# Kernel tuning notes

Measured on AMD Instinct MI355X. Metric: run time of the kernel, lower is better.

## Reference

```python
import jax, jax.numpy as jnp
import numpy as np

B, T, C = 2, 2048, 1024
NUM_HEADS, NUM_KV_HEADS, HEAD_DIM = 16, 8, 64
R = NUM_HEADS // NUM_KV_HEADS  # q heads per kv head
WINDOW = 512
HIDDEN = 4096
SOFT_CAP = 50.0


def setup_inputs() -> dict:
    key = jax.random.key(0)
    ks = jax.random.split(key, 10)
    std = 0.02
    return {
        "x": jax.random.normal(ks[0], (B, T, C), jnp.float32),
        "kurtosis_sum": jnp.zeros((), jnp.float32),
        "rms1_scale": jnp.zeros((C,), jnp.float32),
        "q_kernel": std * jax.random.normal(ks[1], (C, R, NUM_KV_HEADS, HEAD_DIM), jnp.float32),
        "k_kernel": std * jax.random.normal(ks[2], (C, NUM_KV_HEADS, HEAD_DIM), jnp.float32),
        "v_kernel": std * jax.random.normal(ks[3], (C, NUM_KV_HEADS, HEAD_DIM), jnp.float32),
        "out_kernel": std * jax.random.normal(ks[4], (R, NUM_KV_HEADS, HEAD_DIM, C), jnp.float32),
        "rms2_scale": jnp.zeros((C,), jnp.float32),
        "gate_kernel": std * jax.random.normal(ks[5], (C, HIDDEN), jnp.float32),
        "up_kernel": std * jax.random.normal(ks[6], (C, HIDDEN), jnp.float32),
        "down_kernel": std * jax.random.normal(ks[7], (HIDDEN, C), jnp.float32),
    }


def sine_table(features, length, max_timescale=1e6):
    fraction = jnp.arange(0, features, 2, dtype=jnp.float32) / features
    rot_freq = 1.0 / (max_timescale ** fraction)
    sinusoid = jnp.arange(length, dtype=jnp.float32)[:, None] * rot_freq[None, :]
    sinusoid = jnp.concatenate([sinusoid, sinusoid], axis=-1)  # (T, features)
    return jnp.sin(sinusoid), jnp.cos(sinusoid)


def rotate_half(x):
    x1, x2 = jnp.split(x, 2, axis=-1)
    return jnp.concatenate([-x2, x1], axis=-1)


def rms_norm(x, scale):
    var = jnp.mean(jnp.square(x.astype(jnp.float32)), axis=-1, keepdims=True)
    normed = (x * jax.lax.rsqrt(var + 1e-6)).astype(x.dtype)
    return normed * (1 + scale)


def excess_kurtosis(emb):
    mean = jnp.mean(emb, axis=-1, keepdims=True)
    std = jnp.std(emb, axis=-1, keepdims=True)
    centralized = emb - mean
    fourth = jnp.mean(centralized ** 4, axis=-1, keepdims=True)
    kurt = jnp.squeeze(fourth / (std ** 4 + 1e-6), axis=-1).reshape(-1) - 3
    return jnp.sum(jnp.maximum(kurt, 0.0))


def reference(x, kurtosis_sum, rms1_scale, q_kernel, k_kernel, v_kernel,
              out_kernel, rms2_scale, gate_kernel, up_kernel, down_kernel):
    Bc, Tc, Cc = x.shape
    # sliding-window causal mask: j <= i and |i - j| < WINDOW
    idx = jnp.arange(Tc)
    causal = idx[:, None] >= idx[None, :]
    band = jnp.abs(idx[:, None] - idx[None, :]) < WINDOW
    mask = (causal & band)[None, None, None]  # (1,1,1,T,T) for brhsd scores

    # --- attention ---
    attn_in = rms_norm(x, rms1_scale)
    q = jnp.einsum('bsm,mrhk->brhsk', attn_in, q_kernel)
    k = jnp.einsum('bdm,mhk->bhdk', attn_in, k_kernel)
    v = jnp.einsum('bdm,mhv->bhdv', attn_in, v_kernel)

    sin, cos = sine_table(HEAD_DIM, Tc, max_timescale=1e6)
    q = q * cos[None, None, None] + rotate_half(q) * sin[None, None, None]
    k = k * cos[None, None] + rotate_half(k) * sin[None, None]

    scale = jax.lax.rsqrt(jnp.asarray(HEAD_DIM, dtype=x.dtype))
    qk = jnp.einsum('brhsk,bhdk->brhsd', q, k) * scale
    qk = jnp.tanh(qk / SOFT_CAP) * SOFT_CAP
    probs = jax.nn.softmax(qk.astype(jnp.float32), where=mask).astype(x.dtype)
    qkv = jnp.einsum('brhsd,bhdv->brhsv', probs, v)
    attn_out = jnp.einsum('brhsv,rhvm->bsm', qkv, out_kernel)
    x = x + attn_out

    # --- SwiGLU MLP ---
    mlp_in = rms_norm(x, rms2_scale)
    gate = jax.nn.silu(mlp_in @ gate_kernel)
    up = mlp_in @ up_kernel
    x = x + (up * gate) @ down_kernel

    return (x, kurtosis_sum + excess_kurtosis(x))
```

## Files before the change

### kernel.cpp

```cpp
#include <hip/hip_runtime.h>
#include <hip/hip_bf16.h>

typedef __attribute__((ext_vector_type(8))) short short8;
typedef __attribute__((ext_vector_type(4))) float f32x4;
typedef __attribute__((ext_vector_type(4))) int int4v;
typedef __attribute__((ext_vector_type(8))) int int8v;

#define DEVFN static __device__ __forceinline__

DEVFN float bf2f(unsigned short u) {
    unsigned int i = ((unsigned int)u) << 16;
    float f; __builtin_memcpy(&f, &i, 4); return f;
}
DEVFN unsigned short f2bf(float f) {
    unsigned int i; __builtin_memcpy(&i, &f, 4);
    unsigned int r = i + 0x7fffu + ((i >> 16) & 1u);
    return (unsigned short)(r >> 16);
}
DEVFN unsigned char f2fp8(float f) {
    int r = __builtin_amdgcn_cvt_pk_fp8_f32(f, f, 0, false);
    return (unsigned char)(r & 0xff);
}
DEVFN float fastrcp(float x) { return __builtin_amdgcn_rcpf(x); }

DEVFN void load_lds16(const void* g, void* l) {
    __builtin_amdgcn_global_load_lds(
        (__attribute__((address_space(1))) void*)g,
        (__attribute__((address_space(3))) void*)l, 16, 0, 0);
}

DEVFN f32x4 mfma_fp8(int8v a, int8v b, f32x4 c) {
    return __builtin_amdgcn_mfma_scale_f32_16x16x128_f8f6f4(
        a, b, c, 0, 0, 0, 0x7F7F7F7F, 0, 0x7F7F7F7F);
}

constexpr int Bsz = 2, T = 2048, C = 1024;
constexpr int NH = 16, NKV = 8, HD = 64;
constexpr int HID = 4096;
constexpr int NTOK = Bsz * T;
constexpr size_t MiB = 1024 * 1024;

constexpr size_t OFF_WQKV = 0;
constexpr size_t OFF_WOUT = 4 * MiB;
constexpr size_t OFF_WGATE = 6 * MiB;
constexpr size_t OFF_WUP = 10 * MiB;
constexpr size_t OFF_WDOWN = 14 * MiB;
constexpr size_t OFF_XN1 = 18 * MiB;
constexpr size_t OFF_VBUF = 26 * MiB;
constexpr size_t OFF_P2 = 26 * MiB;
constexpr size_t OFF_QB = 58 * MiB;
constexpr size_t OFF_KB = 66 * MiB;
constexpr size_t OFF_VT = 70 * MiB;
constexpr size_t OFF_CTX = 74 * MiB;
constexpr size_t OFF_X2 = 82 * MiB;
constexpr size_t OFF_XN2 = 98 * MiB;
constexpr size_t OFF_G = 102 * MiB;
constexpr size_t OFF_P4 = 118 * MiB;
constexpr size_t OFF_ST = 134 * MiB;
constexpr size_t OFF_CT = 134 * MiB + 256 * 1024;

__global__ __launch_bounds__(256) void prep_kernel(
    const float* __restrict__ qk, const float* __restrict__ kk2,
    const float* __restrict__ vk, const float* __restrict__ ok,
    const float* __restrict__ gk, const float* __restrict__ uk,
    const float* __restrict__ dk,
    unsigned short* __restrict__ wqkv, unsigned short* __restrict__ wout,
    unsigned char* __restrict__ wgate, unsigned char* __restrict__ wup,
    unsigned char* __restrict__ wdown,
    const float* __restrict__ x, const float* __restrict__ rms1_scale,
    unsigned short* __restrict__ xn1,
    float* __restrict__ st, float* __restrict__ ct) {
    __shared__ float t[32][33];
    __shared__ float red[4];
    int id = blockIdx.x;
    int tid = threadIdx.x;
    if (id >= 19456) {
        int idx = (id - 19456) * 256 + tid;
        float fr = (float)(idx & 31) * (1.f / 32.f);
        float freq = powf(1e6f, -fr);
        float a = (float)(idx >> 5) * freq;
        st[idx] = sinf(a);
        ct[idx] = cosf(a);
        return;
    }
    if (id >= 15360) {
        int row = id - 15360;
        const float4 v = *(const float4*)&x[(size_t)row * 1024 + tid * 4];
        float ss = v.x * v.x + v.y * v.y + v.z * v.z + v.w * v.w;
#pragma unroll
        for (int m = 32; m; m >>= 1) ss += __shfl_xor(ss, m, 64);
        if ((tid & 63) == 0) red[tid >> 6] = ss;
        __syncthreads();
        float tot = red[0] + red[1] + red[2] + red[3];
        float inv = rsqrtf(tot * (1.f / 1024.f) + 1e-6f);
        const float4 sc = *(const float4*)&rms1_scale[tid * 4];
        size_t o = (size_t)row * 1024 + tid * 4;
        xn1[o + 0] = f2bf(v.x * inv * (1.f + sc.x));
        xn1[o + 1] = f2bf(v.y * inv * (1.f + sc.y));
        xn1[o + 2] = f2bf(v.z * inv * (1.f + sc.z));
        xn1[o + 3] = f2bf(v.w * inv * (1.f + sc.w));
        return;
    }
    const float* in; int K, N, nx, base; int fp8 = 0;
    unsigned short* out16 = nullptr; unsigned char* out8 = nullptr;
    if (id < 1024)       { in = qk;  out16 = wqkv;                       K = 1024; N = 1024; nx = 32;  base = 0; }
    else if (id < 1536)  { in = kk2; out16 = wqkv + (size_t)1024 * 1024; K = 1024; N = 512;  nx = 16;  base = 1024; }
    else if (id < 2048)  { in = vk;  out16 = wqkv + (size_t)1536 * 1024; K = 1024; N = 512;  nx = 16;  base = 1536; }
    else if (id < 3072)  { in = ok;  out16 = wout;                       K = 1024; N = 1024; nx = 32;  base = 2048; }
    else if (id < 7168)  { in = gk;  out8 = wgate; fp8 = 1;              K = 1024; N = 4096; nx = 128; base = 3072; }
    else if (id < 11264) { in = uk;  out8 = wup; fp8 = 1;                K = 1024; N = 4096; nx = 128; base = 7168; }
    else                 { in = dk;  out8 = wdown; fp8 = 1;              K = 4096; N = 1024; nx = 32;  base = 11264; }
    int lid = id - base;
    int n0 = (lid % nx) * 32, k0 = (lid / nx) * 32;
    int tx = tid & 31, ty = tid >> 5;
#pragma unroll
    for (int i = 0; i < 4; i++)
        t[ty + 8 * i][tx] = in[(size_t)(k0 + ty + 8 * i) * N + n0 + tx];
    __syncthreads();
    if (fp8) {
#pragma unroll
        for (int i = 0; i < 4; i++)
            out8[(size_t)(n0 + ty + 8 * i) * K + k0 + tx] = f2fp8(t[tx][ty + 8 * i] * 16.f);
    } else {
#pragma unroll
        for (int i = 0; i < 4; i++)
            out16[(size_t)(n0 + ty + 8 * i) * K + k0 + tx] = f2bf(t[tx][ty + 8 * i]);
    }
}

__global__ __launch_bounds__(256) void gemm128(const unsigned short* __restrict__ A,
                                               const unsigned short* __restrict__ Bt,
                                               unsigned short* __restrict__ Cp,
                                               int N, int K, int lda, int ldb,
                                               size_t zA, size_t zB, size_t zC) {
    __shared__ __align__(16) unsigned short As[2][128 * 32];
    __shared__ __align__(16) unsigned short Bs[2][128 * 32];
    A += (size_t)blockIdx.z * zA;
    Bt += (size_t)blockIdx.z * zB;
    const int tid = threadIdx.x;
    const int lane = tid & 63, w = tid >> 6;
    const int quad = lane >> 4, l15 = lane & 15;
    const int wr = w >> 1, wc = w & 1;
    const int m0 = blockIdx.y * 128, n0 = blockIdx.x * 128;

    f32x4 acc[4][4];
#pragma unroll
    for (int i = 0; i < 4; i++)
#pragma unroll
        for (int j = 0; j < 4; j++) acc[i][j] = f32x4{0.f, 0.f, 0.f, 0.f};

    const int stRow = (w << 4) + (lane >> 2);
    const int stCol = (lane & 3) << 3;

    auto STAGE = [&](int kk, int b) {
#pragma unroll
        for (int i = 0; i < 2; i++) {
            load_lds16(A + (size_t)(m0 + (i << 6) + stRow) * lda + kk + stCol,
                       &As[b][((i << 6) + (w << 4)) * 32]);
            load_lds16(Bt + (size_t)(n0 + (i << 6) + stRow) * ldb + kk + stCol,
                       &Bs[b][((i << 6) + (w << 4)) * 32]);
        }
    };

    const int nsteps = K >> 5;
    STAGE(0, 0);
    STAGE(32, 1);
    for (int s = 0; s < nsteps; ++s) {
        if (s < nsteps - 1) asm volatile("s_waitcnt vmcnt(4)\n\ts_barrier" ::: "memory");
        else                asm volatile("s_waitcnt vmcnt(0)\n\ts_barrier" ::: "memory");
        const int b = s & 1;
        short8 a[4], bf[4];
#pragma unroll
        for (int mi = 0; mi < 4; mi++)
            a[mi] = *(const short8*)&As[b][(wr * 64 + mi * 16 + l15) * 32 + quad * 8];
#pragma unroll
        for (int ni = 0; ni < 4; ni++)
            bf[ni] = *(const short8*)&Bs[b][(wc * 64 + ni * 16 + l15) * 32 + quad * 8];
        asm volatile("s_waitcnt lgkmcnt(0)\n\ts_barrier" ::: "memory");
        if (s + 2 < nsteps) STAGE((s + 2) * 32, b);
        __builtin_amdgcn_sched_barrier(0);
        __builtin_amdgcn_s_setprio(1);
#pragma unroll
        for (int mi = 0; mi < 4; mi++)
#pragma unroll
            for (int ni = 0; ni < 4; ni++)
                acc[mi][ni] = __builtin_amdgcn_mfma_f32_16x16x32_bf16(a[mi], bf[ni], acc[mi][ni], 0, 0, 0);
        __builtin_amdgcn_s_setprio(0);
    }
#pragma unroll
    for (int mi = 0; mi < 4; mi++)
#pragma unroll
        for (int ni = 0; ni < 4; ni++)
#pragma unroll
            for (int r = 0; r < 4; r++) {
                int row = m0 + wr * 64 + mi * 16 + quad * 4 + r;
                int col = n0 + wc * 64 + ni * 16 + l15;
                Cp[(size_t)blockIdx.z * zC + (size_t)row * N + col] = f2bf(acc[mi][ni][r]);
            }
}

__global__ __launch_bounds__(256) void gemm_qkv(const unsigned short* __restrict__ A,
                                                const unsigned short* __restrict__ Bt,
                                                unsigned short* __restrict__ qb,
                                                unsigned short* __restrict__ kb,
                                                unsigned short* __restrict__ vbuf,
                                                const float* __restrict__ st,
                                                const float* __restrict__ ct) {
    __shared__ __align__(16) unsigned short As[2][128 * 32];
    __shared__ __align__(16) unsigned short Bs[2][128 * 32];
    const int tid = threadIdx.x;
    const int lane = tid & 63, w = tid >> 6;
    const int quad = lane >> 4, l15 = lane & 15;
    const int wr = w >> 1, wc = w & 1;
    const int m0 = blockIdx.y * 128, n0 = blockIdx.x * 128;

    f32x4 acc[4][4];
#pragma unroll
    for (int i = 0; i < 4; i++)
#pragma unroll
        for (int j = 0; j < 4; j++) acc[i][j] = f32x4{0.f, 0.f, 0.f, 0.f};

    const int stRow = (w << 4) + (lane >> 2);
    const int stCol = (lane & 3) << 3;

    auto STAGE = [&](int kk, int b) {
#pragma unroll
        for (int i = 0; i < 2; i++) {
            load_lds16(A + (size_t)(m0 + (i << 6) + stRow) * 1024 + kk + stCol,
                       &As[b][((i << 6) + (w << 4)) * 32]);
            load_lds16(Bt + (size_t)(n0 + (i << 6) + stRow) * 1024 + kk + stCol,
                       &Bs[b][((i << 6) + (w << 4)) * 32]);
        }
    };

    STAGE(0, 0);
    STAGE(32, 1);
    for (int s = 0; s < 32; ++s) {
        if (s < 31) asm volatile("s_waitcnt vmcnt(4)\n\ts_barrier" ::: "memory");
        else        asm volatile("s_waitcnt vmcnt(0)\n\ts_barrier" ::: "memory");
        const int b = s & 1;
        short8 a[4], bf[4];
#pragma unroll
        for (int mi = 0; mi < 4; mi++)
            a[mi] = *(const short8*)&As[b][(wr * 64 + mi * 16 + l15) * 32 + quad * 8];
#pragma unroll
        for (int ni = 0; ni < 4; ni++)
            bf[ni] = *(const short8*)&Bs[b][(wc * 64 + ni * 16 + l15) * 32 + quad * 8];
        asm volatile("s_waitcnt lgkmcnt(0)\n\ts_barrier" ::: "memory");
        if (s < 30) STAGE((s + 2) * 32, b);
        __builtin_amdgcn_sched_barrier(0);
        __builtin_amdgcn_s_setprio(1);
#pragma unroll
        for (int mi = 0; mi < 4; mi++)
#pragma unroll
            for (int ni = 0; ni < 4; ni++)
                acc[mi][ni] = __builtin_amdgcn_mfma_f32_16x16x32_bf16(a[mi], bf[ni], acc[mi][ni], 0, 0, 0);
        __builtin_amdgcn_s_setprio(0);
    }

    if (n0 < 1536) {
        const int head = (n0 + wc * 64) >> 6;
        const bool isq = head < 16;
        unsigned short* ob = isq ? qb : kb;
        const int hb = isq ? head : head - 16;
        const int hn = isq ? 16 : 8;
#pragma unroll
        for (int ni = 0; ni < 2; ni++) {
            const int d = ni * 16 + l15;
#pragma unroll
            for (int mi = 0; mi < 4; mi++)
#pragma unroll
                for (int r = 0; r < 4; r++) {
                    int row = m0 + wr * 64 + mi * 16 + quad * 4 + r;
                    int t = row & 2047, bb = row >> 11;
                    float c = ct[t * 32 + d], sv = st[t * 32 + d];
                    float x1 = acc[mi][ni][r], x2 = acc[mi][ni + 2][r];
                    size_t obase = ((size_t)(bb * hn + hb) * 2048 + t) * 64;
                    ob[obase + d]      = f2bf(x1 * c - x2 * sv);
                    ob[obase + d + 32] = f2bf(x2 * c + x1 * sv);
                }
        }
    } else {
#pragma unroll
        for (int mi = 0; mi < 4; mi++)
#pragma unroll
            for (int ni = 0; ni < 4; ni++)
#pragma unroll
                for (int r = 0; r < 4; r++) {
                    int row = m0 + wr * 64 + mi * 16 + quad * 4 + r;
                    int col = n0 - 1536 + wc * 64 + ni * 16 + l15;
                    vbuf[(size_t)row * 512 + col] = f2bf(acc[mi][ni][r]);
                }
    }
}

__global__ __launch_bounds__(256) void vtrans_kernel(const unsigned short* __restrict__ vbuf,
                                                     unsigned short* __restrict__ vt) {
    __shared__ unsigned short tile[64][68];
    int lid = blockIdx.x;
    int tid = threadIdx.x;
    int b = lid >> 8, h = (lid >> 5) & 7, t0 = (lid & 31) * 64;
    int d = tid & 63, tr = tid >> 6;
#pragma unroll
    for (int i = 0; i < 16; i++) {
        int t = tr + i * 4;
        tile[t][d] = vbuf[(size_t)(b * 2048 + t0 + t) * 512 + h * 64 + d];
    }
    __syncthreads();
    int tt = tid & 63, dr = tid >> 6;
#pragma unroll
    for (int i = 0; i < 16; i++) {
        int dd = dr + i * 4;
        vt[((size_t)(b * 8 + h) * 64 + dd) * 2048 + t0 + tt] = tile[tt][dd];
    }
}

DEVFN int8v read_frag8(const unsigned char* buf, int rb, int quad) {
    int base = rb * 128;
    int h0 = (2 * quad) ^ (rb & 7);
    int h1 = (2 * quad + 1) ^ (rb & 7);
    int4v lo = *(const int4v*)&buf[base + h0 * 16];
    int4v hi = *(const int4v*)&buf[base + h1 * 16];
    return int8v{lo.x, lo.y, lo.z, lo.w, hi.x, hi.y, hi.z, hi.w};
}

__global__ __launch_bounds__(256) void gateup_kernel(const unsigned char* __restrict__ A,
                                                     const unsigned char* __restrict__ Bg,
                                                     const unsigned char* __restrict__ Bu,
                                                     unsigned char* __restrict__ out) {
    __shared__ __align__(16) unsigned char As[2][128 * 128];
    __shared__ __align__(16) unsigned char Gs[2][64 * 128];
    __shared__ __align__(16) unsigned char Us[2][64 * 128];
    const int tid = threadIdx.x;
    const int lane = tid & 63, w = tid >> 6;
    const int quad = lane >> 4, l15 = lane & 15;
    const int wr = w >> 1, wc = w & 1;
    const int m0 = blockIdx.y * 128, n0 = blockIdx.x * 64;

    f32x4 aG[4][2], aU[4][2];
#pragma unroll
    for (int i = 0; i < 4; i++)
#pragma unroll
        for (int j = 0; j < 2; j++) { aG[i][j] = f32x4{0.f, 0.f, 0.f, 0.f}; aU[i][j] = f32x4{0.f, 0.f, 0.f, 0.f}; }

    const int lrow = lane >> 3;
    const int hA = (lane & 7) ^ lrow;

    auto STAGE = [&](int t, int b) {
#pragma unroll
        for (int j = 0; j < 4; j++) {
            int i = w * 4 + j;
            int r = i * 8 + lrow;
            load_lds16(A + (size_t)(m0 + r) * 1024 + t * 128 + hA * 16, &As[b][i * 1024]);
        }
#pragma unroll
        for (int j = 0; j < 2; j++) {
            int i = w * 2 + j;
            int r = i * 8 + lrow;
            load_lds16(Bg + (size_t)(n0 + r) * 1024 + t * 128 + hA * 16, &Gs[b][i * 1024]);
            load_lds16(Bu + (size_t)(n0 + r) * 1024 + t * 128 + hA * 16, &Us[b][i * 1024]);
        }
    };

    STAGE(0, 0);
    STAGE(1, 1);

#pragma unroll
    for (int t = 0; t < 8; ++t) {
        if (t < 7) asm volatile("s_waitcnt vmcnt(8)\n\ts_barrier" ::: "memory");
        else       asm volatile("s_waitcnt vmcnt(0)\n\ts_barrier" ::: "memory");
        const int b = t & 1;
        int8v a[4], bg[2], bu[2];
#pragma unroll
        for (int mi = 0; mi < 4; mi++)
            a[mi] = read_frag8(As[b], wr * 64 + mi * 16 + l15, quad);
#pragma unroll
        for (int ni = 0; ni < 2; ni++) {
            bg[ni] = read_frag8(Gs[b], wc * 32 + ni * 16 + l15, quad);
            bu[ni] = read_frag8(Us[b], wc * 32 + ni * 16 + l15, quad);
        }
        asm volatile("s_waitcnt lgkmcnt(0)\n\ts_barrier" ::: "memory");
        if (t < 6) STAGE(t + 2, b);
        __builtin_amdgcn_sched_barrier(0);
        __builtin_amdgcn_s_setprio(1);
#pragma unroll
        for (int mi = 0; mi < 4; mi++)
#pragma unroll
            for (int ni = 0; ni < 2; ni++) {
                aG[mi][ni] = mfma_fp8(a[mi], bg[ni], aG[mi][ni]);
                aU[mi][ni] = mfma_fp8(a[mi], bu[ni], aU[mi][ni]);
            }
        __builtin_amdgcn_s_setprio(0);
    }
#pragma unroll
    for (int mi = 0; mi < 4; mi++)
#pragma unroll
        for (int ni = 0; ni < 2; ni++)
#pragma unroll
            for (int r = 0; r < 4; r++) {
                int row = m0 + wr * 64 + mi * 16 + quad * 4 + r;
                int col = n0 + wc * 32 + ni * 16 + l15;
                float vg = aG[mi][ni][r] * (1.f / 64.f);
                float vu = aU[mi][ni][r] * (1.f / 64.f);
                float s = vg * fastrcp(1.f + __expf(-vg));
                out[(size_t)row * 4096 + col] = f2fp8(s * vu * 8.f);
            }
}

__global__ __launch_bounds__(256) void down_gemm(const unsigned char* __restrict__ A,
                                                 const unsigned char* __restrict__ Bt,
                                                 unsigned short* __restrict__ Cp) {
    __shared__ __align__(16) unsigned char As[2][128 * 128];
    __shared__ __align__(16) unsigned char Bs[2][128 * 128];
    const int tid = threadIdx.x;
    const int lane = tid & 63, w = tid >> 6;
    const int quad = lane >> 4, l15 = lane & 15;
    const int wr = w >> 1, wc = w & 1;
    const int m0 = blockIdx.y * 128, n0 = blockIdx.x * 128;
    const int kbase = blockIdx.z * 2048;

    f32x4 acc[4][4];
#pragma unroll
    for (int i = 0; i < 4; i++)
#pragma unroll
        for (int j = 0; j < 4; j++) acc[i][j] = f32x4{0.f, 0.f, 0.f, 0.f};

    const int lrow = lane >> 3;
    const int hA = (lane & 7) ^ lrow;

    auto STAGE = [&](int t, int b) {
#pragma unroll
        for (int j = 0; j < 4; j++) {
            int i = w * 4 + j;
            int r = i * 8 + lrow;
            load_lds16(A + (size_t)(m0 + r) * 4096 + kbase + t * 128 + hA * 16, &As[b][i * 1024]);
            load_lds16(Bt + (size_t)(n0 + r) * 4096 + kbase + t * 128 + hA * 16, &Bs[b][i * 1024]);
        }
    };

    STAGE(0, 0);
    STAGE(1, 1);

#pragma unroll
    for (int t = 0; t < 16; ++t) {
        if (t < 15) asm volatile("s_waitcnt vmcnt(8)\n\ts_barrier" ::: "memory");
        else        asm volatile("s_waitcnt vmcnt(0)\n\ts_barrier" ::: "memory");
        const int b = t & 1;
        int8v a[4], bb[4];
#pragma unroll
        for (int mi = 0; mi < 4; mi++)
            a[mi] = read_frag8(As[b], wr * 64 + mi * 16 + l15, quad);
#pragma unroll
        for (int ni = 0; ni < 4; ni++)
            bb[ni] = read_frag8(Bs[b], wc * 64 + ni * 16 + l15, quad);
        asm volatile("s_waitcnt lgkmcnt(0)\n\ts_barrier" ::: "memory");
        if (t < 14) STAGE(t + 2, b);
        __builtin_amdgcn_sched_barrier(0);
        __builtin_amdgcn_s_setprio(1);
#pragma unroll
        for (int mi = 0; mi < 4; mi++)
#pragma unroll
            for (int ni = 0; ni < 4; ni++)
                acc[mi][ni] = mfma_fp8(a[mi], bb[ni], acc[mi][ni]);
        __builtin_amdgcn_s_setprio(0);
    }
    const size_t Z = (size_t)NTOK * 1024;
#pragma unroll
    for (int mi = 0; mi < 4; mi++)
#pragma unroll
        for (int ni = 0; ni < 4; ni++)
#pragma unroll
            for (int r = 0; r < 4; r++) {
                int row = m0 + wr * 64 + mi * 16 + quad * 4 + r;
                int col = n0 + wc * 64 + ni * 16 + l15;
                Cp[(size_t)blockIdx.z * Z + (size_t)row * 1024 + col] =
                    f2bf(acc[mi][ni][r] * (1.f / 128.f));
            }
}

__global__ __launch_bounds__(256) void reduce_out(const unsigned short* __restrict__ p,
                                                  const float* __restrict__ x,
                                                  const float* __restrict__ scale,
                                                  float* __restrict__ x2,
                                                  unsigned char* __restrict__ xn2,
                                                  const float* __restrict__ ksum,
                                                  float* __restrict__ outk) {
    __shared__ float red[4];
    int row = blockIdx.x, tid = threadIdx.x;
    if (row == 0 && tid == 0) outk[0] = ksum[0];
    size_t base = (size_t)row * 1024 + tid * 4;
    const size_t Z = (size_t)NTOK * 1024;
    float4 v = *(const float4*)&x[base];
#pragma unroll
    for (int z = 0; z < 2; z++) {
        ushort4 u = *(const ushort4*)&p[base + z * Z];
        v.x += bf2f(u.x); v.y += bf2f(u.y); v.z += bf2f(u.z); v.w += bf2f(u.w);
    }
    *(float4*)&x2[base] = v;
    float ss = v.x * v.x + v.y * v.y + v.z * v.z + v.w * v.w;
#pragma unroll
    for (int m = 32; m; m >>= 1) ss += __shfl_xor(ss, m, 64);
    if ((tid & 63) == 0) red[tid >> 6] = ss;
    __syncthreads();
    float tot = red[0] + red[1] + red[2] + red[3];
    float inv = rsqrtf(tot * (1.f / 1024.f) + 1e-6f) * 4.f;
    const float4 sc = *(const float4*)&scale[tid * 4];
    xn2[base + 0] = f2fp8(v.x * inv * (1.f + sc.x));
    xn2[base + 1] = f2fp8(v.y * inv * (1.f + sc.y));
    xn2[base + 2] = f2fp8(v.z * inv * (1.f + sc.z));
    xn2[base + 3] = f2fp8(v.w * inv * (1.f + sc.w));
}

__global__ __launch_bounds__(256) void reduce_down(const unsigned short* __restrict__ p,
                                                   const float* __restrict__ x2,
                                                   float* __restrict__ outx,
                                                   float* __restrict__ outk) {
    __shared__ float red[4], r2[4], r4[4];
    int row = blockIdx.x, tid = threadIdx.x;
    size_t base = (size_t)row * 1024 + tid * 4;
    const size_t Z = (size_t)NTOK * 1024;
    float4 v = *(const float4*)&x2[base];
#pragma unroll
    for (int z = 0; z < 2; z++) {
        ushort4 u = *(const ushort4*)&p[base + z * Z];
        v.x += bf2f(u.x); v.y += bf2f(u.y); v.z += bf2f(u.z); v.w += bf2f(u.w);
    }
    *(float4*)&outx[base] = v;
    float s = v.x + v.y + v.z + v.w;
#pragma unroll
    for (int m = 32; m; m >>= 1) s += __shfl_xor(s, m, 64);
    if ((tid & 63) == 0) red[tid >> 6] = s;
    __syncthreads();
    float mean = (red[0] + red[1] + red[2] + red[3]) * (1.f / 1024.f);
    float cx = v.x - mean, cy = v.y - mean, cz = v.z - mean, cw = v.w - mean;
    float x2v = cx * cx, y2 = cy * cy, z2 = cz * cz, w2 = cw * cw;
    float c2 = x2v + y2 + z2 + w2;
    float c4 = x2v * x2v + y2 * y2 + z2 * z2 + w2 * w2;
#pragma unroll
    for (int m = 32; m; m >>= 1) {
        c2 += __shfl_xor(c2, m, 64);
        c4 += __shfl_xor(c4, m, 64);
    }
    if ((tid & 63) == 0) { r2[tid >> 6] = c2; r4[tid >> 6] = c4; }
    __syncthreads();
    if (tid == 0) {
        float m2 = (r2[0] + r2[1] + r2[2] + r2[3]) * (1.f / 1024.f);
        float m4 = (r4[0] + r4[1] + r4[2] + r4[3]) * (1.f / 1024.f);
        float kurt = m4 / (m2 * m2 + 1e-6f) - 3.f;
        if (kurt > 0.f) atomicAdd(outk, kurt);
    }
}

__global__ __launch_bounds__(256) void attn_kernel(const unsigned short* __restrict__ qb,
                                                   const unsigned short* __restrict__ kb,
                                                   const unsigned short* __restrict__ vt,
                                                   unsigned short* __restrict__ ctx) {
    __shared__ __align__(16) unsigned short Ks[64 * 64];
    __shared__ __align__(16) unsigned short Vs[64 * 64];
    __shared__ __align__(16) unsigned short P[4][2][16 * 64];
    const int tid = threadIdx.x, lane = tid & 63, w = tid >> 6;
    const int quad = lane >> 4, l15 = lane & 15;
    const int qt = blockIdx.x, H = blockIdx.y, b = blockIdx.z;
    const int hkv = H & 7;
    const int qw = qt * 64 + w * 16;

    const unsigned short* qbase = qb + ((size_t)(b * 16 + H) * 2048 + qw) * 64;
    short8 aq0 = *(const short8*)(qbase + (size_t)l15 * 64 + quad * 8);
    short8 aq1 = *(const short8*)(qbase + (size_t)l15 * 64 + 32 + quad * 8);

    const unsigned short* kbase = kb + (size_t)(b * 8 + hkv) * 2048 * 64;
    const unsigned short* vbase = vt + (size_t)(b * 8 + hkv) * 64 * 2048;

    const short bf1 = (short)0x3F80;
    const short8 ones = {bf1, bf1, bf1, bf1, bf1, bf1, bf1, bf1};

    f32x4 O[4];
#pragma unroll
    for (int i = 0; i < 4; i++) O[i] = f32x4{0.f, 0.f, 0.f, 0.f};
    f32x4 lacc = f32x4{0.f, 0.f, 0.f, 0.f};

    const int srow = lane >> 3;
    const int schunk = (lane & 7) ^ srow;
    const int sw = l15 & 7;

    int kstartB = qt * 64 - 511;
    if (kstartB < 0) kstartB = 0;
    kstartB &= ~63;
    const int kendB = qt * 64 + 63;
    int buf = 0;

    for (int k0 = kstartB; k0 <= kendB; k0 += 64) {
#pragma unroll
        for (int rr = 0; rr < 2; rr++) {
            int row = w * 8 + rr * 32 + srow;
            load_lds16(kbase + (size_t)(k0 + row) * 64 + schunk * 8,
                       &Ks[(w * 8 + rr * 32) * 64]);
            load_lds16(vbase + (size_t)row * 2048 + k0 + schunk * 8,
                       &Vs[(w * 8 + rr * 32) * 64]);
        }
        __syncthreads();
        f32x4 S[4];
#pragma unroll
        for (int c = 0; c < 4; c++) {
            const unsigned short* kp = &Ks[(c * 16 + l15) * 64];
            short8 kf0 = *(const short8*)&kp[(quad ^ sw) * 8];
            short8 kf1 = *(const short8*)&kp[((4 + quad) ^ sw) * 8];
            f32x4 s = __builtin_amdgcn_mfma_f32_16x16x32_bf16(aq0, kf0, f32x4{0.f, 0.f, 0.f, 0.f}, 0, 0, 0);
            s = __builtin_amdgcn_mfma_f32_16x16x32_bf16(aq1, kf1, s, 0, 0, 0);
            S[c] = s;
        }
        unsigned short* Pw = P[w][buf];
#pragma unroll
        for (int c = 0; c < 4; c++)
#pragma unroll
            for (int r = 0; r < 4; r++) {
                int i = qw + quad * 4 + r;
                int j = k0 + c * 16 + l15;
                float Sc = fminf(3200.f, fmaxf(-3200.f, S[c][r]));
                float e = __expf(Sc * 0.005f);
                float y = 50.f - 100.f * fastrcp(e + 1.f);
                bool ok = (j <= i) && ((i - j) < 512);
                float pv = ok ? __expf(y) : 0.f;
                Pw[(quad * 4 + r) * 64 + c * 16 + l15] = f2bf(pv);
            }
        asm volatile("s_waitcnt lgkmcnt(0)" ::: "memory");
        short8 pf0 = *(const short8*)&Pw[l15 * 64 + quad * 8];
        short8 pf1 = *(const short8*)&Pw[l15 * 64 + 32 + quad * 8];
#pragma unroll
        for (int ni = 0; ni < 4; ni++) {
            const unsigned short* vp = &Vs[(ni * 16 + l15) * 64];
            short8 vf0 = *(const short8*)&vp[(quad ^ sw) * 8];
            short8 vf1 = *(const short8*)&vp[((4 + quad) ^ sw) * 8];
            O[ni] = __builtin_amdgcn_mfma_f32_16x16x32_bf16(pf0, vf0, O[ni], 0, 0, 0);
            O[ni] = __builtin_amdgcn_mfma_f32_16x16x32_bf16(pf1, vf1, O[ni], 0, 0, 0);
        }
        lacc = __builtin_amdgcn_mfma_f32_16x16x32_bf16(pf0, ones, lacc, 0, 0, 0);
        lacc = __builtin_amdgcn_mfma_f32_16x16x32_bf16(pf1, ones, lacc, 0, 0, 0);
        buf ^= 1;
        __syncthreads();
    }
#pragma unroll
    for (int r = 0; r < 4; r++) {
        float inv = fastrcp(lacc[r]);
        int i = qw + quad * 4 + r;
        size_t tok = (size_t)b * 2048 + i;
#pragma unroll
        for (int ni = 0; ni < 4; ni++)
            ctx[tok * 1024 + H * 64 + ni * 16 + l15] = f2bf(O[ni][r] * inv);
    }
}

extern "C" void kernel_launch(void* const* d_in, const int* in_sizes, int n_in,
                              void* d_out, int out_size, void* d_ws, size_t ws_size,
                              hipStream_t stream) {
    const float* x = (const float*)d_in[0];
    const float* ksum = (const float*)d_in[1];
    const float* rms1_scale = (const float*)d_in[2];
    const float* q_w = (const float*)d_in[3];
    const float* k_w = (const float*)d_in[4];
    const float* v_w = (const float*)d_in[5];
    const float* out_w = (const float*)d_in[6];
    const float* rms2_scale = (const float*)d_in[7];
    const float* gate_w = (const float*)d_in[8];
    const float* up_w = (const float*)d_in[9];
    const float* down_w = (const float*)d_in[10];

    char* ws = (char*)d_ws;
    unsigned short* wqkv = (unsigned short*)(ws + OFF_WQKV);
    unsigned short* wout = (unsigned short*)(ws + OFF_WOUT);
    unsigned char* wgate = (unsigned char*)(ws + OFF_WGATE);
    unsigned char* wup = (unsigned char*)(ws + OFF_WUP);
    unsigned char* wdown = (unsigned char*)(ws + OFF_WDOWN);
    unsigned short* xn1 = (unsigned short*)(ws + OFF_XN1);
    unsigned short* vbuf = (unsigned short*)(ws + OFF_VBUF);
    unsigned short* p2 = (unsigned short*)(ws + OFF_P2);
    unsigned short* qb = (unsigned short*)(ws + OFF_QB);
    unsigned short* kb = (unsigned short*)(ws + OFF_KB);
    unsigned short* vtb = (unsigned short*)(ws + OFF_VT);
    unsigned short* ctx = (unsigned short*)(ws + OFF_CTX);
    float* x2 = (float*)(ws + OFF_X2);
    unsigned char* xn2 = (unsigned char*)(ws + OFF_XN2);
    unsigned char* g = (unsigned char*)(ws + OFF_G);
    unsigned short* p4 = (unsigned short*)(ws + OFF_P4);
    float* st = (float*)(ws + OFF_ST);
    float* ct = (float*)(ws + OFF_CT);
    float* outx = (float*)d_out;
    float* outk = outx + (size_t)NTOK * C;

    prep_kernel<<<19712, 256, 0, stream>>>(
        q_w, k_w, v_w, out_w, gate_w, up_w, down_w,
        wqkv, wout, wgate, wup, wdown, x, rms1_scale, xn1, st, ct);

    gemm_qkv<<<dim3(2048 / 128, NTOK / 128), 256, 0, stream>>>(
        xn1, wqkv, qb, kb, vbuf, st, ct);

    vtrans_kernel<<<512, 256, 0, stream>>>(vbuf, vtb);

    attn_kernel<<<dim3(T / 64, NH, Bsz), 256, 0, stream>>>(qb, kb, vtb, ctx);

    gemm128<<<dim3(1024 / 128, NTOK / 128, 2), 256, 0, stream>>>(
        ctx, wout, p2, 1024, 512, 1024, 1024, 512, 512, (size_t)NTOK * 1024);
    reduce_out<<<NTOK, 256, 0, stream>>>(p2, x, rms2_scale, x2, xn2, ksum, outk);

    gateup_kernel<<<dim3(HID / 64, NTOK / 128), 256, 0, stream>>>(xn2, wgate, wup, g);

    down_gemm<<<dim3(1024 / 128, NTOK / 128, 2), 256, 0, stream>>>(g, wdown, p4);
    reduce_down<<<NTOK, 256, 0, stream>>>(p4, x2, outx, outk);

    (void)in_sizes; (void)n_in; (void)out_size; (void)ws_size;
}
```

Measured before the change: 314.2 us.

## Widen gate/up GEMM tile to 128 columns, single-buffer LDS, vectorize weight prep

The gate/up FP8 GEMM now computes a 128x128 output tile per block instead of 128x64, doubling accumulators and halving the grid. To fit LDS it drops double buffering in favour of a single buffer and adds a launch bound of two blocks per CU. The goal is more reuse of each A tile across more output columns. The trade-off is that loads for the next K step are exposed, since they now wait on vmcnt(0) each iteration. The prep transpose kernel also switches to float4 loads and 4-wide packed stores to cut memory transactions.

```diff
diff --git a/kernel.cpp b/kernel.cpp
--- a/kernel.cpp
+++ b/kernel.cpp
@@ -112,19 +112,27 @@
     else                 { in = dk;  out8 = wdown; fp8 = 1;              K = 4096; N = 1024; nx = 32;  base = 11264; }
     int lid = id - base;
     int n0 = (lid % nx) * 32, k0 = (lid / nx) * 32;
-    int tx = tid & 31, ty = tid >> 5;
-#pragma unroll
-    for (int i = 0; i < 4; i++)
-        t[ty + 8 * i][tx] = in[(size_t)(k0 + ty + 8 * i) * N + n0 + tx];
+    {
+        int r = tid >> 3, c4 = (tid & 7) * 4;
+        const float4 v = *(const float4*)&in[(size_t)(k0 + r) * N + n0 + c4];
+        t[r][c4 + 0] = v.x; t[r][c4 + 1] = v.y; t[r][c4 + 2] = v.z; t[r][c4 + 3] = v.w;
+    }
     __syncthreads();
+    int nr = tid >> 3, kc4 = (tid & 7) * 4;
     if (fp8) {
-#pragma unroll
-        for (int i = 0; i < 4; i++)
-            out8[(size_t)(n0 + ty + 8 * i) * K + k0 + tx] = f2fp8(t[tx][ty + 8 * i] * 16.f);
+        uchar4 o;
+        o.x = f2fp8(t[kc4 + 0][nr] * 16.f);
+        o.y = f2fp8(t[kc4 + 1][nr] * 16.f);
+        o.z = f2fp8(t[kc4 + 2][nr] * 16.f);
+        o.w = f2fp8(t[kc4 + 3][nr] * 16.f);
+        *(uchar4*)&out8[(size_t)(n0 + nr) * K + k0 + kc4] = o;
     } else {
-#pragma unroll
-        for (int i = 0; i < 4; i++)
-            out16[(size_t)(n0 + ty + 8 * i) * K + k0 + tx] = f2bf(t[tx][ty + 8 * i]);
+        ushort4 o;
+        o.x = f2bf(t[kc4 + 0][nr]);
+        o.y = f2bf(t[kc4 + 1][nr]);
+        o.z = f2bf(t[kc4 + 2][nr]);
+        o.w = f2bf(t[kc4 + 3][nr]);
+        *(ushort4*)&out16[(size_t)(n0 + nr) * K + k0 + kc4] = o;
     }
 }
 
@@ -324,69 +332,61 @@
     return int8v{lo.x, lo.y, lo.z, lo.w, hi.x, hi.y, hi.z, hi.w};
 }
 
-__global__ __launch_bounds__(256) void gateup_kernel(const unsigned char* __restrict__ A,
-                                                     const unsigned char* __restrict__ Bg,
-                                                     const unsigned char* __restrict__ Bu,
-                                                     unsigned char* __restrict__ out) {
-    __shared__ __align__(16) unsigned char As[2][128 * 128];
-    __shared__ __align__(16) unsigned char Gs[2][64 * 128];
-    __shared__ __align__(16) unsigned char Us[2][64 * 128];
+__global__ __launch_bounds__(256, 2) void gateup_kernel(const unsigned char* __restrict__ A,
+                                                        const unsigned char* __restrict__ Bg,
+                                                        const unsigned char* __restrict__ Bu,
+                                                        unsigned char* __restrict__ out) {
+    __shared__ __align__(16) unsigned char As[128 * 128];
+    __shared__ __align__(16) unsigned char Gs[128 * 128];
+    __shared__ __align__(16) unsigned char Us[128 * 128];
     const int tid = threadIdx.x;
     const int lane = tid & 63, w = tid >> 6;
     const int quad = lane >> 4, l15 = lane & 15;
     const int wr = w >> 1, wc = w & 1;
-    const int m0 = blockIdx.y * 128, n0 = blockIdx.x * 64;
-
-    f32x4 aG[4][2], aU[4][2];
+    const int m0 = blockIdx.y * 128, n0 = blockIdx.x * 128;
+
+    f32x4 aG[4][4], aU[4][4];
 #pragma unroll
     for (int i = 0; i < 4; i++)
 #pragma unroll
-        for (int j = 0; j < 2; j++) { aG[i][j] = f32x4{0.f, 0.f, 0.f, 0.f}; aU[i][j] = f32x4{0.f, 0.f, 0.f, 0.f}; }
+        for (int j = 0; j < 4; j++) { aG[i][j] = f32x4{0.f, 0.f, 0.f, 0.f}; aU[i][j] = f32x4{0.f, 0.f, 0.f, 0.f}; }
 
     const int lrow = lane >> 3;
     const int hA = (lane & 7) ^ lrow;
 
-    auto STAGE = [&](int t, int b) {
+    auto STAGE = [&](int t) {
 #pragma unroll
         for (int j = 0; j < 4; j++) {
             int i = w * 4 + j;
             int r = i * 8 + lrow;
-            load_lds16(A + (size_t)(m0 + r) * 1024 + t * 128 + hA * 16, &As[b][i * 1024]);
-        }
-#pragma unroll
-        for (int j = 0; j < 2; j++) {
-            int i = w * 2 + j;
-            int r = i * 8 + lrow;
-            load_lds16(Bg + (size_t)(n0 + r) * 1024 + t * 128 + hA * 16, &Gs[b][i * 1024]);
-            load_lds16(Bu + (size_t)(n0 + r) * 1024 + t * 128 + hA * 16, &Us[b][i * 1024]);
+            load_lds16(A  + (size_t)(m0 + r) * 1024 + t * 128 + hA * 16, &As[i * 1024]);
+            load_lds16(Bg + (size_t)(n0 + r) * 1024 + t * 128 + hA * 16, &Gs[i * 1024]);
+            load_lds16(Bu + (size_t)(n0 + r) * 1024 + t * 128 + hA * 16, &Us[i * 1024]);
         }
     };
 
-    STAGE(0, 0);
-    STAGE(1, 1);
+    STAGE(0);
 
 #pragma unroll
     for (int t = 0; t < 8; ++t) {
-        if (t < 7) asm volatile("s_waitcnt vmcnt(8)\n\ts_barrier" ::: "memory");
-        else       asm volatile("s_waitcnt vmcnt(0)\n\ts_barrier" ::: "memory");
-        const int b = t & 1;
-        int8v a[4], bg[2], bu[2];
-#pragma unroll
-        for (int mi = 0; mi < 4; mi++)
-            a[mi] = read_frag8(As[b], wr * 64 + mi * 16 + l15, quad);
-#pragma unroll
-        for (int ni = 0; ni < 2; ni++) {
-            bg[ni] = read_frag8(Gs[b], wc * 32 + ni * 16 + l15, quad);
-            bu[ni] = read_frag8(Us[b], wc * 32 + ni * 16 + l15, quad);
+        asm volatile("s_waitcnt vmcnt(0)\n\ts_barrier" ::: "memory");
+        int8v a[4], bg[4], bu[4];
+#pragma unroll
+        for (int mi = 0; mi < 4; mi++)
+            a[mi] = read_frag8(As, wr * 64 + mi * 16 + l15, quad);
+#pragma unroll
+        for (int ni = 0; ni < 4; ni++) {
+            bg[ni] = read_frag8(Gs, wc * 64 + ni * 16 + l15, quad);
+            bu[ni] = read_frag8(Us, wc * 64 + ni * 16 + l15, quad);
         }
         asm volatile("s_waitcnt lgkmcnt(0)\n\ts_barrier" ::: "memory");
-        if (t < 6) STAGE(t + 2, b);
+        if (t < 7) STAGE(t + 1);
         __builtin_amdgcn_sched_barrier(0);
         __builtin_amdgcn_s_setprio(1);
 #pragma unroll
         for (int mi = 0; mi < 4; mi++)
 #pragma unroll
-            for (int ni = 0; ni < 2; ni++) {
+            for (int ni = 0; ni < 4; ni++) {
                 aG[mi][ni] = mfma_fp8(a[mi], bg[ni], aG[mi][ni]);
                 aU[mi][ni] = mfma_fp8(a[mi], bu[ni], aU[mi][ni]);
             }
@@ -395,11 +395,11 @@
 #pragma unroll
     for (int mi = 0; mi < 4; mi++)
 #pragma unroll
-        for (int ni = 0; ni < 2; ni++)
+        for (int ni = 0; ni < 4; ni++)
 #pragma unroll
             for (int r = 0; r < 4; r++) {
                 int row = m0 + wr * 64 + mi * 16 + quad * 4 + r;
-                int col = n0 + wc * 32 + ni * 16 + l15;
+                int col = n0 + wc * 64 + ni * 16 + l15;
                 float vg = aG[mi][ni][r] * (1.f / 64.f);
                 float vu = aU[mi][ni][r] * (1.f / 64.f);
                 float s = vg * fastrcp(1.f + __expf(-vg));
@@ -702,7 +702,7 @@
         ctx, wout, p2, 1024, 512, 1024, 1024, 512, 512, (size_t)NTOK * 1024);
     reduce_out<<<NTOK, 256, 0, stream>>>(p2, x, rms2_scale, x2, xn2, ksum, outk);
 
-    gateup_kernel<<<dim3(HID / 64, NTOK / 128), 256, 0, stream>>>(xn2, wgate, wup, g);
+    gateup_kernel<<<dim3(HID / 128, NTOK / 128), 256, 0, stream>>>(xn2, wgate, wup, g);
 
     down_gemm<<<dim3(1024 / 128, NTOK / 128, 2), 256, 0, stream>>>(g, wdown, p4);
     reduce_down<<<NTOK, 256, 0, stream>>>(p4, x2, outx, outk);
```

Result: slower. 334.4 us (+6.4%).

## Fuse V transpose into QKV GEMM epilogue and vectorize weight prep

Applied to the files above, without the earlier changes.

The QKV GEMM now writes the V projection straight into the transposed per-head layout the attention kernel expects. It stages the tile through a padded shared-memory buffer and stores 16-byte chunks, which removes the separate vtrans kernel launch and its round trip through global memory. The weight-prep kernel also switches to float4 loads and 4-wide packed stores. The cost is extra shared memory in gemm_qkv, which may lower occupancy, plus additional barriers in the V-block epilogue.

```diff
diff --git a/kernel.cpp b/kernel.cpp
--- a/kernel.cpp
+++ b/kernel.cpp
@@ -46,7 +46,6 @@
 constexpr size_t OFF_WUP = 10 * MiB;
 constexpr size_t OFF_WDOWN = 14 * MiB;
 constexpr size_t OFF_XN1 = 18 * MiB;
-constexpr size_t OFF_VBUF = 26 * MiB;
 constexpr size_t OFF_P2 = 26 * MiB;
 constexpr size_t OFF_QB = 58 * MiB;
 constexpr size_t OFF_KB = 66 * MiB;
@@ -112,19 +111,27 @@
     else                 { in = dk;  out8 = wdown; fp8 = 1;              K = 4096; N = 1024; nx = 32;  base = 11264; }
     int lid = id - base;
     int n0 = (lid % nx) * 32, k0 = (lid / nx) * 32;
-    int tx = tid & 31, ty = tid >> 5;
-#pragma unroll
-    for (int i = 0; i < 4; i++)
-        t[ty + 8 * i][tx] = in[(size_t)(k0 + ty + 8 * i) * N + n0 + tx];
+    {
+        int r = tid >> 3, c4 = (tid & 7) * 4;
+        const float4 v = *(const float4*)&in[(size_t)(k0 + r) * N + n0 + c4];
+        t[r][c4 + 0] = v.x; t[r][c4 + 1] = v.y; t[r][c4 + 2] = v.z; t[r][c4 + 3] = v.w;
+    }
     __syncthreads();
+    int nr = tid >> 3, kc4 = (tid & 7) * 4;
     if (fp8) {
-#pragma unroll
-        for (int i = 0; i < 4; i++)
-            out8[(size_t)(n0 + ty + 8 * i) * K + k0 + tx] = f2fp8(t[tx][ty + 8 * i] * 16.f);
+        uchar4 o;
+        o.x = f2fp8(t[kc4 + 0][nr] * 16.f);
+        o.y = f2fp8(t[kc4 + 1][nr] * 16.f);
+        o.z = f2fp8(t[kc4 + 2][nr] * 16.f);
+        o.w = f2fp8(t[kc4 + 3][nr] * 16.f);
+        *(uchar4*)&out8[(size_t)(n0 + nr) * K + k0 + kc4] = o;
     } else {
-#pragma unroll
-        for (int i = 0; i < 4; i++)
-            out16[(size_t)(n0 + ty + 8 * i) * K + k0 + tx] = f2bf(t[tx][ty + 8 * i]);
+        ushort4 o;
+        o.x = f2bf(t[kc4 + 0][nr]);
+        o.y = f2bf(t[kc4 + 1][nr]);
+        o.z = f2bf(t[kc4 + 2][nr]);
+        o.w = f2bf(t[kc4 + 3][nr]);
+        *(ushort4*)&out16[(size_t)(n0 + nr) * K + k0 + kc4] = o;
     }
 }
 
@@ -203,11 +210,12 @@
                                                 const unsigned short* __restrict__ Bt,
                                                 unsigned short* __restrict__ qb,
                                                 unsigned short* __restrict__ kb,
-                                                unsigned short* __restrict__ vbuf,
+                                                unsigned short* __restrict__ vt,
                                                 const float* __restrict__ st,
                                                 const float* __restrict__ ct) {
     __shared__ __align__(16) unsigned short As[2][128 * 32];
     __shared__ __align__(16) unsigned short Bs[2][128 * 32];
+    __shared__ __align__(16) unsigned short vtile[2][64][136];
     const int tid = threadIdx.x;
     const int lane = tid & 63, w = tid >> 6;
     const int quad = lane >> 4, l15 = lane & 15;
@@ -281,37 +289,32 @@
                 }
         }
     } else {
-#pragma unroll
-        for (int mi = 0; mi < 4; mi++)
-#pragma unroll
-            for (int ni = 0; ni < 4; ni++)
+        __syncthreads();
+#pragma unroll
+        for (int mi = 0; mi < 4; mi++)
+#pragma unroll
+            for (int ni = 0; ni < 4; ni++) {
+                const int d = ni * 16 + l15;
 #pragma unroll
                 for (int r = 0; r < 4; r++) {
-                    int row = m0 + wr * 64 + mi * 16 + quad * 4 + r;
-                    int col = n0 - 1536 + wc * 64 + ni * 16 + l15;
-                    vbuf[(size_t)row * 512 + col] = f2bf(acc[mi][ni][r]);
+                    int tokloc = wr * 64 + mi * 16 + quad * 4 + r;
+                    vtile[wc][d][tokloc] = f2bf(acc[mi][ni][r]);
                 }
-    }
-}
-
-__global__ __launch_bounds__(256) void vtrans_kernel(const unsigned short* __restrict__ vbuf,
-                                                     unsigned short* __restrict__ vt) {
-    __shared__ unsigned short tile[64][68];
-    int lid = blockIdx.x;
-    int tid = threadIdx.x;
-    int b = lid >> 8, h = (lid >> 5) & 7, t0 = (lid & 31) * 64;
-    int d = tid & 63, tr = tid >> 6;
-#pragma unroll
-    for (int i = 0; i < 16; i++) {
-        int t = tr + i * 4;
-        tile[t][d] = vbuf[(size_t)(b * 2048 + t0 + t) * 512 + h * 64 + d];
-    }
-    __syncthreads();
-    int tt = tid & 63, dr = tid >> 6;
-#pragma unroll
-    for (int i = 0; i < 16; i++) {
-        int dd = dr + i * 4;
-        vt[((size_t)(b * 8 + h) * 64 + dd) * 2048 + t0 + tt] = tile[tt][dd];
+            }
+        __syncthreads();
+        const int hvb = (n0 - 1536) >> 6;
+        const int bb = m0 >> 11;
+        const int tokbase = m0 & 2047;
+#pragma unroll
+        for (int it = 0; it < 8; ++it) {
+            int c = it * 256 + tid;
+            int row = c >> 4;
+            int hh = row >> 6, d = row & 63;
+            int tokc = (c & 15) * 8;
+            short8 val = *(const short8*)&vtile[hh][d][tokc];
+            size_t dst = ((size_t)(bb * 8 + hvb + hh) * 64 + d) * 2048 + tokbase + tokc;
+            *(short8*)&vt[dst] = val;
+        }
     }
 }
 
@@ -672,7 +675,6 @@
     unsigned char* wup = (unsigned char*)(ws + OFF_WUP);
     unsigned char* wdown = (unsigned char*)(ws + OFF_WDOWN);
     unsigned short* xn1 = (unsigned short*)(ws + OFF_XN1);
-    unsigned short* vbuf = (unsigned short*)(ws + OFF_VBUF);
     unsigned short* p2 = (unsigned short*)(ws + OFF_P2);
     unsigned short* qb = (unsigned short*)(ws + OFF_QB);
     unsigned short* kb = (unsigned short*)(ws + OFF_KB);
@@ -692,9 +694,7 @@
         wqkv, wout, wgate, wup, wdown, x, rms1_scale, xn1, st, ct);
 
     gemm_qkv<<<dim3(2048 / 128, NTOK / 128), 256, 0, stream>>>(
-        xn1, wqkv, qb, kb, vbuf, st, ct);
-
-    vtrans_kernel<<<512, 256, 0, stream>>>(vbuf, vtb);
+        xn1, wqkv, qb, kb, vtb, st, ct);
 
     attn_kernel<<<dim3(T / 64, NH, Bsz), 256, 0, stream>>>(qb, kb, vtb, ctx);
 
```

Result: no change. 311.6 us (-0.8%).
